# Kernel optimization log

Hardware: AMD Instinct MI355X
Metric: run time of the kernel (lower is better)

## Reference

```python
import jax, jax.numpy as jnp
import numpy as np

N_HEAD = 16
N_EMBD = 2048
B, S = 2, 2048


def setup_inputs() -> dict:
    key = jax.random.key(0)
    k1, k2, k3 = jax.random.split(key, 3)
    scale = 0.02
    return {
        "hidden_states": jax.random.normal(k1, (B, S, N_EMBD), dtype=jnp.float32),
        "attention_mask": jnp.ones((B, S), dtype=jnp.float32),
        "w_attn": jax.random.normal(k2, (N_EMBD, 3 * N_EMBD), dtype=jnp.float32) * scale,
        "b_attn": jnp.zeros((3 * N_EMBD,), dtype=jnp.float32),
        "w_proj": jax.random.normal(k3, (N_EMBD, N_EMBD), dtype=jnp.float32) * scale,
        "b_proj": jnp.zeros((N_EMBD,), dtype=jnp.float32),
    }


def reference(hidden_states, attention_mask, w_attn, b_attn, w_proj, b_proj):
    b, s, d = hidden_states.shape
    h = N_HEAD
    dh = d // h
    qkv = hidden_states @ w_attn + b_attn          # [b, s, 3d]
    q, k, v = jnp.split(qkv, 3, axis=-1)
    # [b, s, d] -> [b, h, s, dh]
    q = q.reshape(b, s, h, dh).transpose(0, 2, 1, 3)
    k = k.reshape(b, s, h, dh).transpose(0, 2, 1, 3)
    v = v.reshape(b, s, h, dh).transpose(0, 2, 1, 3)
    scores = jnp.einsum("bhqd,bhkd->bhqk", q, k) / jnp.sqrt(jnp.float32(dh))
    # padding mask: [b, s] -> additive bias [b, 1, 1, s]
    bias = (1.0 - attention_mask)[:, None, None, :] * -10000.0
    attn = jax.nn.softmax(scores + bias, axis=-1)   # dropout p=0 (eval)
    out = jnp.einsum("bhqk,bhkd->bhqd", attn, v)    # [b, h, s, dh]
    out = out.transpose(0, 2, 1, 3).reshape(b, s, d)
    return out @ w_proj + b_proj
```

## Files before the change

### kernel.cpp

```cpp
#include <hip/hip_runtime.h>
#include <stdint.h>

#define B_   2
#define S_   2048
#define D_   2048
#define NH_  16
#define DH_  128
#define N3_  6144

typedef unsigned short u16;
typedef __bf16 bf16x8 __attribute__((ext_vector_type(8)));
typedef float  f32x4  __attribute__((ext_vector_type(4)));

#define QSCALE   (0.08838834764831845f * 1.4426950408889634f)
#define BIASF    (-10000.0f * 1.4426950408889634f)

__device__ __forceinline__ u16 f2bf(float f) {
  union { float f; unsigned u; } v; v.f = f;
  unsigned u = v.u;
  return (u16)((u + 0x7FFFu + ((u >> 16) & 1u)) >> 16);
}

__device__ __forceinline__ float fast_exp2(float x) {
  float r;
  asm("v_exp_f32 %0, %1" : "=v"(r) : "v"(x));
  return r;
}

#define GL2LDS(gsrc, ldst)                                                              \
  __builtin_amdgcn_global_load_lds((const __attribute__((address_space(1))) void*)(gsrc), \
      (__attribute__((address_space(3))) void*)(ldst), 16, 0, 0)

__device__ __forceinline__ int swz_id() {
  int id = blockIdx.y * gridDim.x + blockIdx.x;
  int cpx = (gridDim.x * gridDim.y) >> 3;
  return (id & 7) * cpx + (id >> 3);
}

__global__ void cvt_kernel(const float* __restrict__ in, u16* __restrict__ out, int n4) {
  int i = blockIdx.x * blockDim.x + threadIdx.x;
  int stride = gridDim.x * blockDim.x;
  for (; i < n4; i += stride) {
    float4 v = ((const float4*)in)[i];
    ushort4 o;
    o.x = f2bf(v.x); o.y = f2bf(v.y); o.z = f2bf(v.z); o.w = f2bf(v.w);
    ((ushort4*)out)[i] = o;
  }
}

__global__ void transpose_kernel(const float* __restrict__ in, u16* __restrict__ out,
                                 int K, int N) {
  __shared__ float tile[32][33];
  int tx = threadIdx.x, ty = threadIdx.y;
  int nx = blockIdx.x * 32, ky = blockIdx.y * 32;
#pragma unroll
  for (int j = 0; j < 32; j += 8)
    tile[ty + j][tx] = in[(size_t)(ky + ty + j) * N + nx + tx];
  __syncthreads();
#pragma unroll
  for (int j = 0; j < 32; j += 8)
    out[(size_t)(nx + ty + j) * K + ky + tx] = f2bf(tile[tx][ty + j]);
}

template <int KD>
__device__ __forceinline__ void gemm_core(const u16* __restrict__ A,
                                          const u16* __restrict__ BT,
                                          int m0, int n0, u16* As, u16* Bs,
                                          f32x4 acc[4][4]) {
  int t = threadIdx.x;
  int lane = t & 63, wv = t >> 6;
  int g = lane >> 4, lr = lane & 15;
  int wr = wv >> 1, wc = wv & 1;
  for (int k0 = 0; k0 < KD; k0 += 64) {
#pragma unroll
    for (int i = 0; i < 4; ++i) {
      int idx = i * 256 + t;
      int row = idx >> 3, slot = idx & 7;
      GL2LDS(A + (size_t)(m0 + row) * KD + k0 + ((slot ^ (row & 7)) * 8), As + idx * 8);
    }
#pragma unroll
    for (int i = 0; i < 4; ++i) {
      int idx = i * 256 + t;
      int row = idx >> 3, slot = idx & 7;
      GL2LDS(BT + (size_t)(n0 + row) * KD + k0 + ((slot ^ (row & 7)) * 8), Bs + idx * 8);
    }
    __syncthreads();
#pragma unroll
    for (int kk = 0; kk < 2; ++kk) {
      bf16x8 af[4], bfr[4];
#pragma unroll
      for (int m = 0; m < 4; ++m) {
        int r = wr * 64 + m * 16 + lr;
        af[m] = *reinterpret_cast<const bf16x8*>(As + r * 64 + ((((kk << 2) | g) ^ (r & 7)) * 8));
      }
#pragma unroll
      for (int n = 0; n < 4; ++n) {
        int r = wc * 64 + n * 16 + lr;
        bfr[n] = *reinterpret_cast<const bf16x8*>(Bs + r * 64 + ((((kk << 2) | g) ^ (r & 7)) * 8));
      }
#pragma unroll
      for (int m = 0; m < 4; ++m)
#pragma unroll
        for (int n = 0; n < 4; ++n)
          acc[m][n] = __builtin_amdgcn_mfma_f32_16x16x32_bf16(af[m], bfr[n], acc[m][n], 0, 0, 0);
    }
    __syncthreads();
  }
}

__global__ __launch_bounds__(256) void gemm_qkv_kernel(
    const u16* __restrict__ A, const u16* __restrict__ BT, const float* __restrict__ bias,
    u16* __restrict__ Qb, u16* __restrict__ Kb, u16* __restrict__ VTb) {
  __shared__ __attribute__((aligned(16))) u16 As[128 * 64];
  __shared__ __attribute__((aligned(16))) u16 Bs[128 * 64];
  f32x4 acc[4][4] = {};
  int sw = swz_id();
  int n0 = (sw % gridDim.x) * 128, m0 = (sw / gridDim.x) * 128;
  gemm_core<2048>(A, BT, m0, n0, As, Bs, acc);
  int t = threadIdx.x, lane = t & 63, wv = t >> 6;
  int g = lane >> 4, lr = lane & 15, wr = wv >> 1, wc = wv & 1;
#pragma unroll
  for (int m = 0; m < 4; ++m) {
    int rowbase = m0 + wr * 64 + m * 16 + g * 4;
    int b = rowbase >> 11, s = rowbase & 2047;
#pragma unroll
    for (int n = 0; n < 4; ++n) {
      int col = n0 + wc * 64 + n * 16 + lr;
      float bv = bias[col];
      int sec = col >> 11;
      int within = col & 2047;
      int h = within >> 7, d = within & 127;
      if (sec < 2) {
        float mult = (sec == 0) ? QSCALE : 1.0f;
        u16* dst = (sec == 0 ? Qb : Kb) + ((size_t)(b * NH_ + h) * S_ + s) * DH_ + d;
#pragma unroll
        for (int r = 0; r < 4; ++r) dst[(size_t)r * DH_] = f2bf((acc[m][n][r] + bv) * mult);
      } else {
        u16* dst = VTb + ((size_t)(b * NH_ + h) * DH_ + d) * S_ + s;
        ushort4 pk;
        pk.x = f2bf(acc[m][n][0] + bv); pk.y = f2bf(acc[m][n][1] + bv);
        pk.z = f2bf(acc[m][n][2] + bv); pk.w = f2bf(acc[m][n][3] + bv);
        *reinterpret_cast<ushort4*>(dst) = pk;
      }
    }
  }
}

__global__ __launch_bounds__(256) void gemm_proj_kernel(
    const u16* __restrict__ A, const u16* __restrict__ BT, const float* __restrict__ bias,
    float* __restrict__ out) {
  __shared__ __attribute__((aligned(16))) u16 As[128 * 64];
  __shared__ __attribute__((aligned(16))) u16 Bs[128 * 64];
  f32x4 acc[4][4] = {};
  int sw = swz_id();
  int n0 = (sw % gridDim.x) * 128, m0 = (sw / gridDim.x) * 128;
  gemm_core<2048>(A, BT, m0, n0, As, Bs, acc);
  int t = threadIdx.x, lane = t & 63, wv = t >> 6;
  int g = lane >> 4, lr = lane & 15, wr = wv >> 1, wc = wv & 1;
#pragma unroll
  for (int m = 0; m < 4; ++m) {
    int rowbase = m0 + wr * 64 + m * 16 + g * 4;
#pragma unroll
    for (int n = 0; n < 4; ++n) {
      int col = n0 + wc * 64 + n * 16 + lr;
      float bv = bias[col];
      float* dst = out + (size_t)rowbase * D_ + col;
#pragma unroll
      for (int r = 0; r < 4; ++r) dst[(size_t)r * D_] = acc[m][n][r] + bv;
    }
  }
}

__global__ __launch_bounds__(256) void attn_kernel(
    const u16* __restrict__ Qb, const u16* __restrict__ Kb, const u16* __restrict__ VTb,
    const float* __restrict__ mask, u16* __restrict__ AO) {
  __shared__ __attribute__((aligned(16))) u16 Ks[2][64 * 128];
  __shared__ __attribute__((aligned(16))) u16 Vs[2][128 * 64];
  __shared__ __attribute__((aligned(16))) u16 Ps[4][16 * 64];
  __shared__ float bias_lds[S_];

  int t = threadIdx.x, w = t >> 6, lane = t & 63;
  int g = lane >> 4, lr = lane & 15;
  int sw = swz_id();
  int qt = sw & 31, bh = sw >> 5;
  int b = bh >> 4;
  const u16* Qh = Qb + (size_t)bh * S_ * DH_;
  const u16* Kh = Kb + (size_t)bh * S_ * DH_;
  const u16* Vh = VTb + (size_t)bh * DH_ * S_;
  int q0 = qt * 64 + w * 16;

  for (int i = t; i < S_; i += 256)
    bias_lds[i] = (1.0f - mask[b * S_ + i]) * BIASF;

  bf16x8 aq[4];
#pragma unroll
  for (int kk = 0; kk < 4; ++kk)
    aq[kk] = *reinterpret_cast<const bf16x8*>(Qh + (size_t)(q0 + lr) * DH_ + kk * 32 + g * 8);

  f32x4 oacc[8] = {};
  float m_r[4], l_r[4];
#pragma unroll
  for (int r = 0; r < 4; ++r) { m_r[r] = -1e30f; l_r[r] = 0.f; }

  __syncthreads();

#define STAGE_KV(buf, s0base)                                                    \
  {                                                                              \
    _Pragma("unroll")                                                            \
    for (int i = 0; i < 4; ++i) {                                                \
      int idx = i * 256 + t;                                                     \
      int row = idx >> 4, slot = idx & 15;                                       \
      GL2LDS(Kh + (size_t)((s0base) + row) * DH_ + ((slot ^ (row & 7)) * 8),     \
             &Ks[buf][idx * 8]);                                                 \
    }                                                                            \
    _Pragma("unroll")                                                            \
    for (int i = 0; i < 4; ++i) {                                                \
      int idx = i * 256 + t;                                                     \
      int row = idx >> 3, slot = idx & 7;                                        \
      GL2LDS(Vh + (size_t)row * S_ + (s0base) + ((slot ^ (row & 7)) * 8),        \
             &Vs[buf][idx * 8]);                                                 \
    }                                                                            \
  }

  STAGE_KV(0, 0);
  const int NT = S_ / 64;
  for (int it = 0; it < NT; ++it) {
    int cur = it & 1;
    if (it + 1 < NT) {
      STAGE_KV(cur ^ 1, (it + 1) * 64);
      asm volatile("s_waitcnt vmcnt(8)" ::: "memory");
    } else {
      asm volatile("s_waitcnt vmcnt(0)" ::: "memory");
    }
    __builtin_amdgcn_s_barrier();
    __builtin_amdgcn_sched_barrier(0);

    f32x4 sacc[4] = {};
#pragma unroll
    for (int kk = 0; kk < 4; ++kk) {
#pragma unroll
      for (int n = 0; n < 4; ++n) {
        int c = lr + 16 * n;
        bf16x8 bk = *reinterpret_cast<const bf16x8*>(
            &Ks[cur][c * 128 + ((((kk << 2) | g) ^ (c & 7)) * 8)]);
        sacc[n] = __builtin_amdgcn_mfma_f32_16x16x32_bf16(aq[kk], bk, sacc[n], 0, 0, 0);
      }
    }

    int s0 = it * 64;
    float sv[4][4], mx[4];
#pragma unroll
    for (int r = 0; r < 4; ++r) {
#pragma unroll
      for (int n = 0; n < 4; ++n) sv[r][n] = sacc[n][r] + bias_lds[s0 + lr + 16 * n];
      float m2 = fmaxf(fmaxf(sv[r][0], sv[r][1]), fmaxf(sv[r][2], sv[r][3]));
#pragma unroll
      for (int off = 1; off < 16; off <<= 1) m2 = fmaxf(m2, __shfl_xor(m2, off));
      mx[r] = m2;
    }
    float gmax = fmaxf(fmaxf(mx[0] - m_r[0], mx[1] - m_r[1]),
                       fmaxf(mx[2] - m_r[2], mx[3] - m_r[3]));
    if (__any(gmax > 8.f)) {
#pragma unroll
      for (int r = 0; r < 4; ++r) {
        float mnew = fmaxf(m_r[r], mx[r]);
        float f = fast_exp2(m_r[r] - mnew);
        m_r[r] = mnew;
        l_r[r] *= f;
#pragma unroll
        for (int no = 0; no < 8; ++no) oacc[no][r] *= f;
      }
    }
#pragma unroll
    for (int r = 0; r < 4; ++r) {
      int prow = g * 4 + r;
#pragma unroll
      for (int n = 0; n < 4; ++n) {
        float p = fast_exp2(sv[r][n] - m_r[r]);
        l_r[r] += p;
        int col = lr + 16 * n;
        Ps[w][prow * 64 + ((((col >> 3) ^ (prow & 7)) << 3) + (col & 7))] = f2bf(p);
      }
    }

#pragma unroll
    for (int kk2 = 0; kk2 < 2; ++kk2) {
      bf16x8 ap = *reinterpret_cast<const bf16x8*>(
          &Ps[w][lr * 64 + ((((kk2 << 2) | g) ^ (lr & 7)) * 8)]);
#pragma unroll
      for (int no = 0; no < 8; ++no) {
        int d = lr + 16 * no;
        bf16x8 bv = *reinterpret_cast<const bf16x8*>(
            &Vs[cur][d * 64 + ((((kk2 << 2) | g) ^ (d & 7)) * 8)]);
        oacc[no] = __builtin_amdgcn_mfma_f32_16x16x32_bf16(ap, bv, oacc[no], 0, 0, 0);
      }
    }
    __builtin_amdgcn_sched_barrier(0);
    __builtin_amdgcn_s_barrier();
  }
#undef STAGE_KV

#pragma unroll
  for (int r = 0; r < 4; ++r) {
    float s = l_r[r];
#pragma unroll
    for (int off = 1; off < 16; off <<= 1) s += __shfl_xor(s, off);
    float inv = 1.0f / s;
    int qrow = q0 + g * 4 + r;
    int h = bh & 15;
    u16* dst = AO + ((size_t)(b * S_ + qrow)) * D_ + h * DH_;
#pragma unroll
    for (int no = 0; no < 8; ++no) dst[lr + 16 * no] = f2bf(oacc[no][r] * inv);
  }
}

extern "C" void kernel_launch(void* const* d_in, const int* in_sizes, int n_in,
                              void* d_out, int out_size, void* d_ws, size_t ws_size,
                              hipStream_t stream) {
  const float* h_in   = (const float*)d_in[0];
  const float* mask   = (const float*)d_in[1];
  const float* w_attn = (const float*)d_in[2];
  const float* b_attn = (const float*)d_in[3];
  const float* w_proj = (const float*)d_in[4];
  const float* b_proj = (const float*)d_in[5];
  float* out = (float*)d_out;

  char* ws = (char*)d_ws;
  u16* Hb  = (u16*)(ws);
  u16* W1T = (u16*)(ws + 16777216);
  u16* W2T = (u16*)(ws + 41943040);
  u16* Qb  = (u16*)(ws + 50331648);
  u16* Kb  = (u16*)(ws + 67108864);
  u16* VTb = (u16*)(ws + 83886080);
  u16* AO  = Hb;

  cvt_kernel<<<2048, 256, 0, stream>>>(h_in, Hb, (B_ * S_ * D_) / 4);
  dim3 tb(32, 8);
  transpose_kernel<<<dim3(N3_ / 32, D_ / 32), tb, 0, stream>>>(w_attn, W1T, D_, N3_);
  transpose_kernel<<<dim3(D_ / 32, D_ / 32), tb, 0, stream>>>(w_proj, W2T, D_, D_);
  gemm_qkv_kernel<<<dim3(N3_ / 128, (B_ * S_) / 128), 256, 0, stream>>>(
      Hb, W1T, b_attn, Qb, Kb, VTb);
  attn_kernel<<<dim3(S_ / 64, B_ * NH_), 256, 0, stream>>>(Qb, Kb, VTb, mask, AO);
  gemm_proj_kernel<<<dim3(D_ / 128, (B_ * S_) / 128), 256, 0, stream>>>(AO, W2T, b_proj, out);
}
```

Before: 468.2 us.

## Switch projection GEMMs to 256x256 tiles with pipelined double-buffered LDS staging

Replaces the 128x128 single-stage GEMM core with a 512-thread, 256x256-tile core that prefetches two K-steps ahead into double-buffered LDS halves, interleaving fragment reads, async global-to-LDS loads and MFMA quadrants with explicit waitcnt/barrier control and raised wave priority during MFMAs. It targets better operand reuse and hiding of global-load latency in the QKV and output projections. The larger tile reduces the grid to 384 and 128 blocks, which may leave CUs idle or create tail waves, and it raises register pressure.

```diff
diff --git a/kernel.cpp b/kernel.cpp
--- a/kernel.cpp
+++ b/kernel.cpp
@@ -62,70 +62,145 @@
     out[(size_t)(nx + ty + j) * K + ky + tx] = f2bf(tile[tx][ty + j]);
 }
 
+
+__device__ __forceinline__ void read_q(const u16* __restrict__ Ab, const u16* __restrict__ Bb,
+                                       int wrB, int wcB, int g, int lr,
+                                       bf16x8 (&AF)[4][2], bf16x8 (&BF)[2][2]) {
+#pragma unroll
+  for (int i = 0; i < 4; ++i) {
+    int hr = wrB + i * 16 + lr;
+#pragma unroll
+    for (int kk = 0; kk < 2; ++kk)
+      AF[i][kk] = *reinterpret_cast<const bf16x8*>(Ab + hr * 64 + ((((kk << 2) | g) ^ (hr & 7)) * 8));
+  }
+#pragma unroll
+  for (int j = 0; j < 2; ++j) {
+    int hbr = wcB + j * 16 + lr;
+#pragma unroll
+    for (int kk = 0; kk < 2; ++kk)
+      BF[j][kk] = *reinterpret_cast<const bf16x8*>(Bb + hbr * 64 + ((((kk << 2) | g) ^ (hbr & 7)) * 8));
+  }
+}
+
+template <int MS, int NS>
+__device__ __forceinline__ void mfma_q(const bf16x8 (&AF)[4][2], const bf16x8 (&BF)[2][2],
+                                       f32x4 (&acc)[8][4]) {
+  __builtin_amdgcn_s_setprio(1);
+#pragma unroll
+  for (int i = 0; i < 4; ++i)
+#pragma unroll
+    for (int j = 0; j < 2; ++j)
+#pragma unroll
+      for (int kk = 0; kk < 2; ++kk)
+        acc[MS * 4 + i][NS * 2 + j] = __builtin_amdgcn_mfma_f32_16x16x32_bf16(
+            AF[i][kk], BF[j][kk], acc[MS * 4 + i][NS * 2 + j], 0, 0, 0);
+  __builtin_amdgcn_s_setprio(0);
+}
+
 template <int KD>
-__device__ __forceinline__ void gemm_core(const u16* __restrict__ A,
-                                          const u16* __restrict__ BT,
-                                          int m0, int n0, u16* As, u16* Bs,
-                                          f32x4 acc[4][4]) {
-  int t = threadIdx.x;
-  int lane = t & 63, wv = t >> 6;
+__device__ __forceinline__ void stage_a(const u16* __restrict__ A, u16* lds,
+                                        int c, int h, int Tg, int m0, int t) {
+#pragma unroll
+  for (int inst = 0; inst < 2; ++inst) {
+    int idx = inst * 512 + t, hr = idx >> 3, slot = idx & 7;
+    int trow = ((hr >> 6) << 7) + h * 64 + (hr & 63);
+    GL2LDS(A + (size_t)(m0 + trow) * KD + Tg * 64 + ((slot ^ (hr & 7)) * 8),
+           lds + c * 32768 + h * 8192 + idx * 8);
+  }
+}
+
+template <int KD>
+__device__ __forceinline__ void stage_b(const u16* __restrict__ BT, u16* lds,
+                                        int c, int h, int Tg, int n0, int t) {
+#pragma unroll
+  for (int inst = 0; inst < 2; ++inst) {
+    int idx = inst * 512 + t, hr = idx >> 3, slot = idx & 7;
+    int n = ((hr >> 5) << 6) + h * 32 + (hr & 31);
+    GL2LDS(BT + (size_t)(n0 + n) * KD + Tg * 64 + ((slot ^ (hr & 7)) * 8),
+           lds + c * 32768 + 16384 + h * 8192 + idx * 8);
+  }
+}
+
+#define ABASE(c, h) (lds + (c) * 32768 + (h) * 8192)
+#define BBASE(c, h) (lds + (c) * 32768 + 16384 + (h) * 8192)
+#define VMCNT(n) asm volatile("s_waitcnt vmcnt(" #n ")" ::: "memory")
+#define LGKM0                                            \
+  do {                                                   \
+    asm volatile("s_waitcnt lgkmcnt(0)" ::: "memory");   \
+    __builtin_amdgcn_sched_barrier(0);                   \
+  } while (0)
+#define BAR __builtin_amdgcn_s_barrier()
+
+template <int KD>
+__device__ __forceinline__ void gemm256_core(const u16* __restrict__ A, const u16* __restrict__ BT,
+                                             int m0, int n0, u16* lds, f32x4 (&acc)[8][4]) {
+  const int NT = KD / 64;
+  int t = threadIdx.x, wv = t >> 6, lane = t & 63;
   int g = lane >> 4, lr = lane & 15;
-  int wr = wv >> 1, wc = wv & 1;
-  for (int k0 = 0; k0 < KD; k0 += 64) {
-#pragma unroll
-    for (int i = 0; i < 4; ++i) {
-      int idx = i * 256 + t;
-      int row = idx >> 3, slot = idx & 7;
-      GL2LDS(A + (size_t)(m0 + row) * KD + k0 + ((slot ^ (row & 7)) * 8), As + idx * 8);
-    }
-#pragma unroll
-    for (int i = 0; i < 4; ++i) {
-      int idx = i * 256 + t;
-      int row = idx >> 3, slot = idx & 7;
-      GL2LDS(BT + (size_t)(n0 + row) * KD + k0 + ((slot ^ (row & 7)) * 8), Bs + idx * 8);
-    }
-    __syncthreads();
-#pragma unroll
-    for (int kk = 0; kk < 2; ++kk) {
-      bf16x8 af[4], bfr[4];
-#pragma unroll
-      for (int m = 0; m < 4; ++m) {
-        int r = wr * 64 + m * 16 + lr;
-        af[m] = *reinterpret_cast<const bf16x8*>(As + r * 64 + ((((kk << 2) | g) ^ (r & 7)) * 8));
-      }
-#pragma unroll
-      for (int n = 0; n < 4; ++n) {
-        int r = wc * 64 + n * 16 + lr;
-        bfr[n] = *reinterpret_cast<const bf16x8*>(Bs + r * 64 + ((((kk << 2) | g) ^ (r & 7)) * 8));
-      }
-#pragma unroll
-      for (int m = 0; m < 4; ++m)
-#pragma unroll
-        for (int n = 0; n < 4; ++n)
-          acc[m][n] = __builtin_amdgcn_mfma_f32_16x16x32_bf16(af[m], bfr[n], acc[m][n], 0, 0, 0);
-    }
-    __syncthreads();
-  }
-}
-
-__global__ __launch_bounds__(256) void gemm_qkv_kernel(
+  int wrB = (wv >> 2) * 64, wcB = (wv & 3) * 32;
+  bf16x8 af0[4][2], bf0[2][2], af1[4][2], bf1[2][2];
+
+  stage_b<KD>(BT, lds, 0, 0, 0, n0, t);
+  stage_a<KD>(A, lds, 0, 0, 0, m0, t);
+  stage_a<KD>(A, lds, 0, 1, 0, m0, t);
+  stage_b<KD>(BT, lds, 0, 1, 0, n0, t);
+  stage_b<KD>(BT, lds, 1, 0, 1, n0, t);
+  stage_a<KD>(A, lds, 1, 0, 1, m0, t);
+  VMCNT(2);
+  stage_a<KD>(A, lds, 1, 1, 1, m0, t);
+  stage_b<KD>(BT, lds, 1, 1, 1, n0, t);
+  BAR;
+  read_q(ABASE(0, 0), BBASE(0, 0), wrB, wcB, g, lr, af0, bf0);
+  LGKM0;
+
+  for (int T = 0; T < NT; ++T) {
+    int c = T & 1;
+    read_q(ABASE(c, 1), BBASE(c, 0), wrB, wcB, g, lr, af1, bf1);
+    BAR; LGKM0;
+    mfma_q<0, 0>(af0, bf0, acc);
+    BAR;
+    read_q(ABASE(c, 0), BBASE(c, 1), wrB, wcB, g, lr, af0, bf0);
+    if (T + 2 < NT) stage_b<KD>(BT, lds, c, 0, T + 2, n0, t);
+    BAR; LGKM0;
+    mfma_q<1, 0>(af1, bf1, acc);
+    BAR;
+    read_q(ABASE(c, 1), BBASE(c, 1), wrB, wcB, g, lr, af1, bf1);
+    if (T + 2 < NT) stage_a<KD>(A, lds, c, 0, T + 2, m0, t);
+    BAR; LGKM0;
+    mfma_q<0, 1>(af0, bf0, acc);
+    BAR;
+    if (T + 2 < NT) {
+      VMCNT(2);
+      stage_a<KD>(A, lds, c, 1, T + 2, m0, t);
+      stage_b<KD>(BT, lds, c, 1, T + 2, n0, t);
+    } else {
+      VMCNT(0);
+    }
+    BAR;
+    if (T + 1 < NT) read_q(ABASE(c ^ 1, 0), BBASE(c ^ 1, 0), wrB, wcB, g, lr, af0, bf0);
+    LGKM0;
+    mfma_q<1, 1>(af1, bf1, acc);
+    BAR;
+  }
+}
+
+__global__ __launch_bounds__(512, 1) void gemm_qkv_kernel(
     const u16* __restrict__ A, const u16* __restrict__ BT, const float* __restrict__ bias,
     u16* __restrict__ Qb, u16* __restrict__ Kb, u16* __restrict__ VTb) {
-  __shared__ __attribute__((aligned(16))) u16 As[128 * 64];
-  __shared__ __attribute__((aligned(16))) u16 Bs[128 * 64];
-  f32x4 acc[4][4] = {};
+  __shared__ __attribute__((aligned(16))) u16 lds[65536];
+  f32x4 acc[8][4] = {};
   int sw = swz_id();
-  int n0 = (sw % gridDim.x) * 128, m0 = (sw / gridDim.x) * 128;
-  gemm_core<2048>(A, BT, m0, n0, As, Bs, acc);
+  int n0 = (sw % gridDim.x) * 256, m0 = (sw / gridDim.x) * 256;
+  gemm256_core<2048>(A, BT, m0, n0, lds, acc);
   int t = threadIdx.x, lane = t & 63, wv = t >> 6;
-  int g = lane >> 4, lr = lane & 15, wr = wv >> 1, wc = wv & 1;
-#pragma unroll
-  for (int m = 0; m < 4; ++m) {
-    int rowbase = m0 + wr * 64 + m * 16 + g * 4;
+  int g = lane >> 4, lr = lane & 15, wr = wv >> 2, wc = wv & 3;
+#pragma unroll
+  for (int mi = 0; mi < 8; ++mi) {
+    int rowbase = m0 + wr * 128 + mi * 16 + g * 4;
     int b = rowbase >> 11, s = rowbase & 2047;
 #pragma unroll
-    for (int n = 0; n < 4; ++n) {
-      int col = n0 + wc * 64 + n * 16 + lr;
+    for (int nj = 0; nj < 4; ++nj) {
+      int col = n0 + wc * 64 + nj * 16 + lr;
       float bv = bias[col];
       int sec = col >> 11;
       int within = col & 2047;
@@ -134,39 +209,38 @@
         float mult = (sec == 0) ? QSCALE : 1.0f;
         u16* dst = (sec == 0 ? Qb : Kb) + ((size_t)(b * NH_ + h) * S_ + s) * DH_ + d;
 #pragma unroll
-        for (int r = 0; r < 4; ++r) dst[(size_t)r * DH_] = f2bf((acc[m][n][r] + bv) * mult);
+        for (int r = 0; r < 4; ++r) dst[(size_t)r * DH_] = f2bf((acc[mi][nj][r] + bv) * mult);
       } else {
         u16* dst = VTb + ((size_t)(b * NH_ + h) * DH_ + d) * S_ + s;
         ushort4 pk;
-        pk.x = f2bf(acc[m][n][0] + bv); pk.y = f2bf(acc[m][n][1] + bv);
-        pk.z = f2bf(acc[m][n][2] + bv); pk.w = f2bf(acc[m][n][3] + bv);
+        pk.x = f2bf(acc[mi][nj][0] + bv); pk.y = f2bf(acc[mi][nj][1] + bv);
+        pk.z = f2bf(acc[mi][nj][2] + bv); pk.w = f2bf(acc[mi][nj][3] + bv);
         *reinterpret_cast<ushort4*>(dst) = pk;
       }
     }
   }
 }
 
-__global__ __launch_bounds__(256) void gemm_proj_kernel(
+__global__ __launch_bounds__(512, 1) void gemm_proj_kernel(
     const u16* __restrict__ A, const u16* __restrict__ BT, const float* __restrict__ bias,
     float* __restrict__ out) {
-  __shared__ __attribute__((aligned(16))) u16 As[128 * 64];
-  __shared__ __attribute__((aligned(16))) u16 Bs[128 * 64];
-  f32x4 acc[4][4] = {};
+  __shared__ __attribute__((aligned(16))) u16 lds[65536];
+  f32x4 acc[8][4] = {};
   int sw = swz_id();
-  int n0 = (sw % gridDim.x) * 128, m0 = (sw / gridDim.x) * 128;
-  gemm_core<2048>(A, BT, m0, n0, As, Bs, acc);
+  int n0 = (sw % gridDim.x) * 256, m0 = (sw / gridDim.x) * 256;
+  gemm256_core<2048>(A, BT, m0, n0, lds, acc);
   int t = threadIdx.x, lane = t & 63, wv = t >> 6;
-  int g = lane >> 4, lr = lane & 15, wr = wv >> 1, wc = wv & 1;
-#pragma unroll
-  for (int m = 0; m < 4; ++m) {
-    int rowbase = m0 + wr * 64 + m * 16 + g * 4;
-#pragma unroll
-    for (int n = 0; n < 4; ++n) {
-      int col = n0 + wc * 64 + n * 16 + lr;
+  int g = lane >> 4, lr = lane & 15, wr = wv >> 2, wc = wv & 3;
+#pragma unroll
+  for (int mi = 0; mi < 8; ++mi) {
+    int rowbase = m0 + wr * 128 + mi * 16 + g * 4;
+#pragma unroll
+    for (int nj = 0; nj < 4; ++nj) {
+      int col = n0 + wc * 64 + nj * 16 + lr;
       float bv = bias[col];
       float* dst = out + (size_t)rowbase * D_ + col;
 #pragma unroll
-      for (int r = 0; r < 4; ++r) dst[(size_t)r * D_] = acc[m][n][r] + bv;
+      for (int r = 0; r < 4; ++r) dst[(size_t)r * D_] = acc[mi][nj][r] + bv;
     }
   }
 }
@@ -338,8 +412,8 @@
   dim3 tb(32, 8);
   transpose_kernel<<<dim3(N3_ / 32, D_ / 32), tb, 0, stream>>>(w_attn, W1T, D_, N3_);
   transpose_kernel<<<dim3(D_ / 32, D_ / 32), tb, 0, stream>>>(w_proj, W2T, D_, D_);
-  gemm_qkv_kernel<<<dim3(N3_ / 128, (B_ * S_) / 128), 256, 0, stream>>>(
+  gemm_qkv_kernel<<<dim3(N3_ / 256, (B_ * S_) / 256), 512, 0, stream>>>(
       Hb, W1T, b_attn, Qb, Kb, VTb);
   attn_kernel<<<dim3(S_ / 64, B_ * NH_), 256, 0, stream>>>(Qb, Kb, VTb, mask, AO);
-  gemm_proj_kernel<<<dim3(D_ / 128, (B_ * S_) / 128), 256, 0, stream>>>(AO, W2T, b_proj, out);
-}
+  gemm_proj_kernel<<<dim3(D_ / 256, (B_ * S_) / 256), 512, 0, stream>>>(AO, W2T, b_proj, out);
+}
```

After: 488.7 us. 4.4% more time.
